# Optimization experiments

Measured on AMD Instinct MI355X. Metric: run time of the kernel, lower is better.

## Reference

```python
import jax, jax.numpy as jnp
import numpy as np
from jax import lax

H = W = 224
FH = FW = 7          # backbone feature map spatial size
THRESH = 0.7
NUM_CLASSES = 14


def _conv(x, w, stride, pad):
    return lax.conv_general_dilated(
        x, w, (stride, stride), [(pad, pad), (pad, pad)],
        dimension_numbers=('NCHW', 'OIHW', 'NCHW'))


def backbone(x, w0, w1, w2, w3, fw, fb):
    # stand-in resnet50 trunk: 224 -> 56 -> 28 -> 14 -> 7, channels 3->64->512->1024->2048
    h = jax.nn.relu(_conv(x, w0, 4, 3))      # [B,64,56,56]
    h = jax.nn.relu(_conv(h, w1, 2, 1))      # [B,512,28,28]
    h = jax.nn.relu(_conv(h, w2, 2, 1))      # [B,1024,14,14]
    feat = jax.nn.relu(_conv(h, w3, 2, 1))   # [B,2048,7,7]
    pool = feat.max(axis=(2, 3))             # MaxPool2d(k=7,s=1) on 7x7 == global max -> [B,2048]
    out = jax.nn.sigmoid(pool @ fw.T + fb)   # fc + Sigmoid -> [B,14]
    return out, feat, pool


def attention_gen_patchs(img, fm):
    B, C, Hh, Ww = img.shape
    # per-sample channel-max abs heatmap, min-max normalized
    hm = jnp.max(jnp.abs(fm), axis=1)                              # [B,7,7]
    mn = hm.min(axis=(1, 2), keepdims=True)
    mx = hm.max(axis=(1, 2), keepdims=True)
    hm = (hm - mn) / (mx - mn)
    hm = jax.image.resize(hm, (B, Hh, Ww), method='bilinear')      # Resize((h,w))
    mask = (hm > THRESH).astype(jnp.int32)                         # [B,H,W]

    # largest 8-connected component: iterative max-label propagation
    ids = jnp.arange(1, Hh * Ww + 1, dtype=jnp.int32).reshape(1, Hh, Ww) * mask
    def body(_, lab):
        p = lax.reduce_window(lab, jnp.int32(0), lax.max, (1, 3, 3), (1, 1, 1), 'SAME')
        return p * mask
    labels = lax.fori_loop(0, Hh + Ww, body, ids)                  # [B,H,W] int32

    def counts_one(lab):
        c = jnp.zeros((Hh * Ww + 1,), jnp.int32).at[lab.reshape(-1)].add(1)
        return c.at[0].set(-1)                                     # ignore background
    counts = jax.vmap(counts_one)(labels)                          # [B,H*W+1]
    max_label = jnp.argmax(counts, axis=1)                         # [B]
    lcc = labels == max_label[:, None, None]                       # [B,H,W] bool

    # bbox of largest component (xmin/xmax over rows, ymin/ymax over cols)
    ri = jnp.arange(Hh); ci = jnp.arange(Ww)
    rows = lcc.any(axis=2); cols = lcc.any(axis=1)
    xmin = jnp.min(jnp.where(rows, ri[None, :], Hh), axis=1)
    xmax = jnp.max(jnp.where(rows, ri[None, :], -1), axis=1)       # inclusive; torch slice excludes it
    ymin = jnp.min(jnp.where(cols, ci[None, :], Ww), axis=1)
    ymax = jnp.max(jnp.where(cols, ci[None, :], -1), axis=1)
    ch = jnp.maximum(xmax - xmin, 1).astype(jnp.float32)           # crop height (exclusive slice)
    cw = jnp.maximum(ymax - ymin, 1).astype(jnp.float32)

    # bilinear resize of crop [xmin:xmax, ymin:ymax] back to (H,W), align_corners=False
    fy0 = xmin.astype(jnp.float32); fx0 = ymin.astype(jnp.float32)
    oy = (jnp.arange(Hh, dtype=jnp.float32) + 0.5)[None, :] * (ch[:, None] / Hh) + fy0[:, None] - 0.5
    ox = (jnp.arange(Ww, dtype=jnp.float32) + 0.5)[None, :] * (cw[:, None] / Ww) + fx0[:, None] - 0.5
    oy = jnp.clip(oy, fy0[:, None], jnp.maximum(fy0 + ch - 1.0, fy0)[:, None])
    ox = jnp.clip(ox, fx0[:, None], jnp.maximum(fx0 + cw - 1.0, fx0)[:, None])

    def sample_one(im, yy, xx):  # im [C,H,W]
        gy = jnp.broadcast_to(yy[:, None], (Hh, Ww))
        gx = jnp.broadcast_to(xx[None, :], (Hh, Ww))
        f = lambda chan: jax.scipy.ndimage.map_coordinates(chan, [gy, gx], order=1, mode='nearest')
        return jax.vmap(f)(im)
    return jax.vmap(sample_one)(img, oy, ox)                       # [B,C,H,W]


def bce(p, t):
    p = jnp.clip(p, 1e-7, 1.0 - 1e-7)
    return -jnp.mean(t * jnp.log(p) + (1.0 - t) * jnp.log1p(-p))


def setup_inputs() -> dict:
    key = jax.random.key(0)
    ks = jax.random.split(key, 20)
    B = 4
    def conv_w(k, o, i, s):
        return jax.random.normal(k, (o, i, s, s), jnp.float32) * np.sqrt(2.0 / (i * s * s)).astype(np.float32)
    def lin(k, o, i):
        return jax.random.normal(k, (o, i), jnp.float32) * np.sqrt(1.0 / i).astype(np.float32)
    inp = {
        'img': jax.random.uniform(ks[0], (B, 3, H, W), jnp.float32),
        'target': jax.random.uniform(ks[1], (B, NUM_CLASSES), jnp.float32),
        'gw0': conv_w(ks[2], 64, 3, 7), 'gw1': conv_w(ks[3], 512, 64, 3),
        'gw2': conv_w(ks[4], 1024, 512, 3), 'gw3': conv_w(ks[5], 2048, 1024, 3),
        'gfw': lin(ks[6], NUM_CLASSES, 2048), 'gfb': jnp.zeros((NUM_CLASSES,), jnp.float32),
        'lw0': conv_w(ks[7], 64, 3, 7), 'lw1': conv_w(ks[8], 512, 64, 3),
        'lw2': conv_w(ks[9], 1024, 512, 3), 'lw3': conv_w(ks[10], 2048, 1024, 3),
        'lfw': lin(ks[11], NUM_CLASSES, 2048), 'lfb': jnp.zeros((NUM_CLASSES,), jnp.float32),
        'fw': lin(ks[12], NUM_CLASSES, 2048 * 2), 'fb': jnp.zeros((NUM_CLASSES,), jnp.float32),
    }
    return inp


def reference(img, target, gw0, gw1, gw2, gw3, gfw, gfb,
              lw0, lw1, lw2, lw3, lfw, lfb, fw, fb):
    out_g, fm_g, pool_g = backbone(img, gw0, gw1, gw2, gw3, gfw, gfb)
    # patch generation is non-differentiable in the original (CPU/PIL round trip)
    patch = attention_gen_patchs(lax.stop_gradient(img), lax.stop_gradient(fm_g))
    out_l, _, pool_l = backbone(patch, lw0, lw1, lw2, lw3, lfw, lfb)
    out_f = jax.nn.sigmoid(jnp.concatenate([pool_g, pool_l], axis=1) @ fw.T + fb)
    gl = bce(out_g, target); ll = bce(out_l, target); fl = bce(out_f, target)
    loss = 0.8 * gl + 0.1 * ll + 0.1 * fl
    return loss, out_g, out_l, out_f, patch
```

## Files before the change

### kernel.cpp

```cpp
#include <hip/hip_runtime.h>
#include <math.h>

typedef __attribute__((ext_vector_type(8))) short short8m;
typedef __attribute__((ext_vector_type(4))) float f32x4;

__device__ inline unsigned short bf16_trunc(float f) {
  return (unsigned short)(__float_as_uint(f) >> 16);
}
__device__ inline unsigned short bf16_rte(float f) {
  unsigned u = __float_as_uint(f);
  u += 0x7fffu + ((u >> 16) & 1u);
  return (unsigned short)(u >> 16);
}
__device__ inline float bf16_tof(unsigned short h) {
  return __uint_as_float(((unsigned)h) << 16);
}
__device__ inline short8m* ldsPtr(unsigned short* base, int row, int byteInRow) {
  int off = (row * 128 + byteInRow) ^ ((row & 7) << 4);
  return (short8m*)((char*)base + off);
}
__device__ inline void gload16_lds(const void* g, void* d) {
  __builtin_amdgcn_global_load_lds((const __attribute__((address_space(1))) unsigned int*)g,
                                   (__attribute__((address_space(3))) unsigned int*)d, 16, 0, 0);
}

__global__ __launch_bounds__(256) void k_conv7(const float* __restrict__ x,
                                               const float* __restrict__ w,
                                               float* __restrict__ y) {
  __shared__ float ws[147];
  const int boc = blockIdx.y;
  const int oc = boc & 63;
  const int b = boc >> 6;
  for (int i = threadIdx.x; i < 147; i += 256) ws[i] = w[oc * 147 + i];
  __syncthreads();
  int px = blockIdx.x * 256 + threadIdx.x;
  if (px >= 56 * 56) return;
  int oy = px / 56, ox = px % 56;
  int iy0 = oy * 4 - 3, ix0 = ox * 4 - 3;
  float acc = 0.f;
  for (int c = 0; c < 3; ++c) {
    const float* xp = x + ((size_t)(b * 3 + c)) * 224 * 224;
    #pragma unroll
    for (int ky = 0; ky < 7; ++ky) {
      int iy = iy0 + ky;
      if ((unsigned)iy < 224u) {
        #pragma unroll
        for (int kx = 0; kx < 7; ++kx) {
          int ix = ix0 + kx;
          if ((unsigned)ix < 224u)
            acc += xp[iy * 224 + ix] * ws[c * 49 + ky * 7 + kx];
        }
      }
    }
  }
  y[((size_t)boc * 56 + oy) * 56 + ox] = fmaxf(acc, 0.f);
}

__global__ __launch_bounds__(256) void k_padw(const float* __restrict__ w,
                                              float* __restrict__ wp,
                                              int kreal, int ktot, int noc) {
  int i = blockIdx.x * 256 + threadIdx.x;
  if (i >= noc * ktot) return;
  int oc = i / ktot, k = i % ktot;
  wp[i] = (k < kreal) ? w[oc * kreal + k] : 0.f;
}

template <int CIN, int HIN, int WIN, int HOUT, int WOUT, int KH, int KW, int STR, int PAD, int KTOT>
__global__ __launch_bounds__(256) void k_im2col(const float* __restrict__ x,
                                                unsigned short* __restrict__ XgH,
                                                unsigned short* __restrict__ XgM) {
  constexpr int NPX = 4 * HOUT * WOUT;
  constexpr int K8 = KTOT / 8;
  constexpr int KK = KH * KW;
  int u = blockIdx.x * 256 + threadIdx.x;
  int pxin = u & 63;
  int k8 = (u >> 6) % K8;
  int pxblk = (u >> 6) / K8;
  int px = pxblk * 64 + pxin;
  if (px > NPX - 1) px = NPX - 1;
  const int hw = HOUT * WOUT;
  int pbv = px / hw;
  int r = px % hw;
  int py = r / WOUT, pxv = r % WOUT;
  short8m ph, pm;
  #pragma unroll
  for (int i = 0; i < 8; ++i) {
    int k = k8 * 8 + i;
    int ci = k / KK, tap = k - ci * KK;
    float v = 0.f;
    if (ci < CIN) {
      int iy = py * STR - PAD + tap / KW, ix = pxv * STR - PAD + (tap % KW);
      if ((unsigned)iy < (unsigned)HIN && (unsigned)ix < (unsigned)WIN)
        v = x[(((size_t)pbv * CIN + ci) * HIN + iy) * WIN + ix];
    }
    unsigned short hb = bf16_trunc(v);
    unsigned short mb = bf16_rte(v - bf16_tof(hb));
    ph[i] = (short)hb; pm[i] = (short)mb;
  }
  size_t off = (size_t)u * 8;
  *(short8m*)(XgH + off) = ph;
  *(short8m*)(XgM + off) = pm;
}

template <int COUT, int HOUT, int WOUT, int KTOT, int SPLIT>
__global__ __launch_bounds__(256) void k_gemmx(const unsigned short* __restrict__ XgH,
                                               const unsigned short* __restrict__ XgM,
                                               const float* __restrict__ wsrc,
                                               float* __restrict__ part) {
  constexpr int NPX = 4 * HOUT * WOUT;
  constexpr int NPXB = (NPX + 63) / 64;
  constexpr int NOCB = COUT / 64;
  constexpr int NWG = NPXB * NOCB * SPLIT;
  constexpr int KCH = KTOT / SPLIT;
  constexpr int NCH = KCH / 64;
  __shared__ __align__(16) unsigned short XsH[4096];
  __shared__ __align__(16) unsigned short XsM[4096];
  __shared__ __align__(16) unsigned short WsH[4096];
  __shared__ __align__(16) unsigned short WsM[4096];
  __shared__ int pb[64], pyA[64], pxA[64];
  const int tid = threadIdx.x;
  const int flat = blockIdx.x;
  constexpr int q = NWG >> 3, r = NWG & 7;
  const int xc = flat & 7, of = flat >> 3;
  const int work = ((xc < r) ? xc * (q + 1) : r * (q + 1) + (xc - r) * q) + of;
  const int pxblk = work % NPXB;
  const int t2 = work / NPXB;
  const int oc0 = (t2 % NOCB) * 64;
  const int spl = t2 / NOCB;
  if (tid < 64) {
    int p = pxblk * 64 + tid;
    if (p > NPX - 1) p = NPX - 1;
    int hw = HOUT * WOUT;
    pb[tid] = p / hw;
    int rr = p % hw;
    pyA[tid] = rr / WOUT;
    pxA[tid] = rr % WOUT;
  }
  f32x4 acc[4] = {};
  const int l = tid & 63, wv = tid >> 6;
  const int lr = l & 15, lh = l >> 4;
  __syncthreads();
  for (int ch = 0; ch < NCH; ++ch) {
    const int kbase = spl * KCH + ch * 64;
    const size_t tileOff = (size_t)pxblk * KTOT * 64 + (size_t)kbase * 64;
    #pragma unroll
    for (int t = 0; t < 4; ++t) {
      int ins = wv * 4 + t;
      int pl = ins >> 3, ko = ins & 7;
      const unsigned short* g = (pl ? XgM : XgH) + tileOff + ko * 512 + l * 8;
      unsigned short* d = (pl ? XsM : XsH) + ko * 512;
      gload16_lds(g, d);
    }
    #pragma unroll
    for (int j = 0; j < 2; ++j) {
      int c = tid + 256 * j;
      int oc = c >> 3, koct = c & 7;
      const float* wp = wsrc + (size_t)(oc0 + oc) * KTOT + kbase + koct * 8;
      float vv[8];
      *(float4*)&vv[0] = *(const float4*)wp;
      *(float4*)&vv[4] = *(const float4*)(wp + 4);
      short8m ph, pm;
      #pragma unroll
      for (int i = 0; i < 8; ++i) {
        unsigned short hb = bf16_trunc(vv[i]);
        unsigned short mb = bf16_rte(vv[i] - bf16_tof(hb));
        ph[i] = (short)hb; pm[i] = (short)mb;
      }
      *ldsPtr(WsH, oc, koct * 16) = ph;
      *ldsPtr(WsM, oc, koct * 16) = pm;
    }
    __syncthreads();
    #pragma unroll
    for (int ks = 0; ks < 2; ++ks) {
      const int kbyte = ks * 64 + lh * 16;
      short8m aH = *ldsPtr(WsH, wv * 16 + lr, kbyte);
      short8m aM = *ldsPtr(WsM, wv * 16 + lr, kbyte);
      const int xoff = (ks * 4 + lh) * 512;
      #pragma unroll
      for (int g4 = 0; g4 < 4; ++g4) {
        short8m bH = *(const short8m*)(XsH + xoff + (g4 * 16 + lr) * 8);
        short8m bM = *(const short8m*)(XsM + xoff + (g4 * 16 + lr) * 8);
        acc[g4] = __builtin_amdgcn_mfma_f32_16x16x32_bf16(aH, bH, acc[g4], 0, 0, 0);
        acc[g4] = __builtin_amdgcn_mfma_f32_16x16x32_bf16(aH, bM, acc[g4], 0, 0, 0);
        acc[g4] = __builtin_amdgcn_mfma_f32_16x16x32_bf16(aM, bH, acc[g4], 0, 0, 0);
      }
    }
    __syncthreads();
  }
  const size_t N = (size_t)4 * COUT * HOUT * WOUT;
  #pragma unroll
  for (int g4 = 0; g4 < 4; ++g4) {
    int pxl = g4 * 16 + lr;
    int pidx = pxblk * 64 + pxl;
    if (pidx < NPX) {
      #pragma unroll
      for (int rr = 0; rr < 4; ++rr) {
        int ocl = wv * 16 + lh * 4 + rr;
        float v = acc[g4][rr];
        if (SPLIT == 1) v = fmaxf(v, 0.f);
        part[(size_t)spl * N +
             (((size_t)pb[pxl] * COUT + (oc0 + ocl)) * HOUT + pyA[pxl]) * WOUT + pxA[pxl]] = v;
      }
    }
  }
}

template <int CIN, int HIN, int WIN, int COUT, int HOUT, int WOUT, int SPLIT>
__global__ __launch_bounds__(256) void k_convm(const float* __restrict__ x,
                                               const float* __restrict__ wsrc,
                                               float* __restrict__ part) {
  constexpr int NPX = 4 * HOUT * WOUT;
  constexpr int KTOT = (CIN * 9) / SPLIT;
  constexpr int NCH = KTOT / 64;
  __shared__ __align__(16) unsigned short Xs[2][64][64];
  __shared__ __align__(16) unsigned short Wsh[3][64][64];
  __shared__ int pb[64], pyA[64], pxA[64];
  const int tid = threadIdx.x;
  const int oc0 = blockIdx.y * 64, px0 = blockIdx.x * 64;
  const int spl = blockIdx.z;
  const int kg0 = spl * KTOT;
  if (tid < 64) {
    int p = px0 + tid;
    if (p > NPX - 1) p = NPX - 1;
    int hw = HOUT * WOUT;
    pb[tid] = p / hw;
    int r = p % hw;
    pyA[tid] = r / WOUT;
    pxA[tid] = r % WOUT;
  }
  f32x4 acc[4] = {};
  const int l = tid & 63, wv = tid >> 6;
  const int lr = l & 15, lh = l >> 4;
  __syncthreads();
  for (int ch = 0; ch < NCH; ++ch) {
    const int kbase = kg0 + ch * 64;
    #pragma unroll
    for (int j = 0; j < 2; ++j) {
      int c = tid + 256 * j;
      int oc = c >> 3, koct = c & 7;
      const float* wp = wsrc + (size_t)(oc0 + oc) * (CIN * 9) + kbase + koct * 8;
      float vv[8];
      *(float4*)&vv[0] = *(const float4*)wp;
      *(float4*)&vv[4] = *(const float4*)(wp + 4);
      short8m ph, pm, pl2;
      #pragma unroll
      for (int i = 0; i < 8; ++i) {
        unsigned short hb = bf16_trunc(vv[i]);
        float r = vv[i] - bf16_tof(hb);
        unsigned short mb = bf16_rte(r);
        float r2 = r - bf16_tof(mb);
        unsigned short lb = bf16_rte(r2);
        ph[i] = (short)hb; pm[i] = (short)mb; pl2[i] = (short)lb;
      }
      *ldsPtr(&Wsh[0][0][0], oc, koct * 16) = ph;
      *ldsPtr(&Wsh[1][0][0], oc, koct * 16) = pm;
      *ldsPtr(&Wsh[2][0][0], oc, koct * 16) = pl2;
    }
    #pragma unroll
    for (int j = 0; j < 2; ++j) {
      int c = tid + 256 * j;
      int px = c & 63, koct = c >> 6;
      int pbv = pb[px], py = pyA[px], pxv = pxA[px];
      float vv[8];
      #pragma unroll
      for (int i = 0; i < 8; ++i) {
        int k = kbase + koct * 8 + i;
        int ci = k / 9, tap = k - ci * 9;
        int iy = py * 2 - 1 + tap / 3, ix = pxv * 2 - 1 + (tap % 3);
        float v = 0.f;
        if ((unsigned)iy < (unsigned)HIN && (unsigned)ix < (unsigned)WIN)
          v = x[(((size_t)pbv * CIN + ci) * HIN + iy) * WIN + ix];
        vv[i] = v;
      }
      short8m ph, pm;
      #pragma unroll
      for (int i = 0; i < 8; ++i) {
        unsigned short hb = bf16_trunc(vv[i]);
        unsigned short mb = bf16_rte(vv[i] - bf16_tof(hb));
        ph[i] = (short)hb; pm[i] = (short)mb;
      }
      *ldsPtr(&Xs[0][0][0], px, koct * 16) = ph;
      *ldsPtr(&Xs[1][0][0], px, koct * 16) = pm;
    }
    __syncthreads();
    #pragma unroll
    for (int ks = 0; ks < 2; ++ks) {
      const int kbyte = ks * 64 + lh * 16;
      short8m aH = *ldsPtr(&Wsh[0][0][0], wv * 16 + lr, kbyte);
      short8m aM = *ldsPtr(&Wsh[1][0][0], wv * 16 + lr, kbyte);
      short8m aL = *ldsPtr(&Wsh[2][0][0], wv * 16 + lr, kbyte);
      #pragma unroll
      for (int g = 0; g < 4; ++g) {
        short8m bH = *ldsPtr(&Xs[0][0][0], g * 16 + lr, kbyte);
        short8m bM = *ldsPtr(&Xs[1][0][0], g * 16 + lr, kbyte);
        acc[g] = __builtin_amdgcn_mfma_f32_16x16x32_bf16(aH, bH, acc[g], 0, 0, 0);
        acc[g] = __builtin_amdgcn_mfma_f32_16x16x32_bf16(aH, bM, acc[g], 0, 0, 0);
        acc[g] = __builtin_amdgcn_mfma_f32_16x16x32_bf16(aM, bH, acc[g], 0, 0, 0);
        acc[g] = __builtin_amdgcn_mfma_f32_16x16x32_bf16(aM, bM, acc[g], 0, 0, 0);
        acc[g] = __builtin_amdgcn_mfma_f32_16x16x32_bf16(aL, bH, acc[g], 0, 0, 0);
      }
    }
    __syncthreads();
  }
  const size_t N = (size_t)4 * COUT * HOUT * WOUT;
  #pragma unroll
  for (int g = 0; g < 4; ++g) {
    int pxl = g * 16 + lr;
    int pidx = px0 + pxl;
    if (pidx < NPX) {
      #pragma unroll
      for (int r = 0; r < 4; ++r) {
        int ocl = wv * 16 + lh * 4 + r;
        part[(size_t)spl * N +
             (((size_t)pb[pxl] * COUT + (oc0 + ocl)) * HOUT + pyA[pxl]) * WOUT + pxA[pxl]] =
            acc[g][r];
      }
    }
  }
}

template <int SPLIT>
__global__ __launch_bounds__(256) void k_red(const float* __restrict__ part,
                                             float* __restrict__ y, int n) {
  for (int i = blockIdx.x * 256 + threadIdx.x; i < n; i += gridDim.x * 256) {
    float s = 0.f;
    #pragma unroll
    for (int sp = 0; sp < SPLIT; ++sp) s += part[(size_t)sp * n + i];
    y[i] = fmaxf(s, 0.f);
  }
}

__global__ __launch_bounds__(256) void k_pool(const float* __restrict__ feat,
                                              float* __restrict__ pool) {
  int idx = blockIdx.x * 256 + threadIdx.x;
  if (idx >= 8192) return;
  const float* fp = feat + (size_t)idx * 49;
  float m = fp[0];
  #pragma unroll
  for (int i = 1; i < 49; ++i) m = fmaxf(m, fp[i]);
  pool[idx] = m;
}

__global__ __launch_bounds__(256) void k_fcsig(const float* __restrict__ pool,
                                               const float* __restrict__ fw,
                                               const float* __restrict__ fb,
                                               float* __restrict__ outp) {
  __shared__ float red[256];
  const int blk = blockIdx.x;
  const int b = blk / 14, c = blk % 14;
  const int tid = threadIdx.x;
  float s = 0.f;
  for (int k = tid; k < 2048; k += 256) s += pool[b * 2048 + k] * fw[c * 2048 + k];
  red[tid] = s;
  __syncthreads();
  for (int st = 128; st > 0; st >>= 1) {
    if (tid < st) red[tid] += red[tid + st];
    __syncthreads();
  }
  if (tid == 0) outp[b * 14 + c] = 1.f / (1.f + expf(-(red[0] + fb[c])));
}

__global__ __launch_bounds__(256) void k_fcsig2(const float* __restrict__ poolg,
                                                const float* __restrict__ pooll,
                                                const float* __restrict__ fw,
                                                const float* __restrict__ fb,
                                                float* __restrict__ outp) {
  __shared__ float red[256];
  const int blk = blockIdx.x;
  const int b = blk / 14, c = blk % 14;
  const int tid = threadIdx.x;
  const float* w = fw + (size_t)c * 4096;
  float s = 0.f;
  for (int k = tid; k < 2048; k += 256) s += poolg[b * 2048 + k] * w[k];
  for (int k = tid; k < 2048; k += 256) s += pooll[b * 2048 + k] * w[2048 + k];
  red[tid] = s;
  __syncthreads();
  for (int st = 128; st > 0; st >>= 1) {
    if (tid < st) red[tid] += red[tid + st];
    __syncthreads();
  }
  if (tid == 0) outp[blk] = 1.f / (1.f + expf(-(red[0] + fb[c])));
}

__global__ __launch_bounds__(64) void k_loss(const float* __restrict__ target,
                                             float* __restrict__ dout) {
  __shared__ float red[64];
  const int tid = threadIdx.x;
  float term = 0.f;
  if (tid < 56) {
    float t = target[tid];
    float pg = dout[1 + tid], plo = dout[57 + tid], pf = dout[113 + tid];
    auto bce1 = [&](float pp) {
      pp = fminf(fmaxf(pp, 1e-7f), 1.f - 1e-7f);
      return -(t * logf(pp) + (1.f - t) * log1pf(-pp));
    };
    term = (0.8f * bce1(pg) + 0.1f * bce1(plo) + 0.1f * bce1(pf)) * (1.f / 56.f);
  }
  red[tid] = term;
  __syncthreads();
  for (int st = 32; st > 0; st >>= 1) {
    if (tid < st) red[tid] += red[tid + st];
    __syncthreads();
  }
  if (tid == 0) dout[0] = red[0];
}

__global__ __launch_bounds__(256) void k_hm7a(const float* __restrict__ feat,
                                              float* __restrict__ hmr) {
  __shared__ float red[256];
  const int b = blockIdx.x / 49, cell = blockIdx.x % 49;
  const int tid = threadIdx.x;
  float m = 0.f;
  for (int ch = tid; ch < 2048; ch += 256)
    m = fmaxf(m, fabsf(feat[((size_t)b * 2048 + ch) * 49 + cell]));
  red[tid] = m;
  __syncthreads();
  for (int st = 128; st > 0; st >>= 1) {
    if (tid < st) red[tid] = fmaxf(red[tid], red[tid + st]);
    __syncthreads();
  }
  if (tid == 0) hmr[b * 49 + cell] = red[0];
}

__global__ __launch_bounds__(64) void k_hm7b(const float* __restrict__ hmr,
                                             float* __restrict__ hm7) {
  __shared__ float h[49];
  const int b = blockIdx.x, tid = threadIdx.x;
  if (tid < 49) h[tid] = hmr[b * 49 + tid];
  __syncthreads();
  if (tid == 0) {
    float mn = h[0], mx = h[0];
    for (int i = 1; i < 49; ++i) {
      mn = fminf(mn, h[i]);
      mx = fmaxf(mx, h[i]);
    }
    for (int i = 0; i < 49; ++i) hm7[b * 49 + i] = (h[i] - mn) / (mx - mn);
  }
}

#define MAXR 8
#define NRUNS (224 * MAXR)
__global__ __launch_bounds__(256) void k_ccl(const float* __restrict__ hm7, float* __restrict__ bbox) {
  const int b = blockIdx.x, tid = threadIdx.x;
  __shared__ float h7[49];
  __shared__ short rx0[NRUNS], rx1[NRUNS];
  __shared__ short nr[224];
  __shared__ int lab[NRUNS];
  __shared__ int cnt[NRUNS], mid[NRUNS];
  __shared__ int rmn[NRUNS], rmx[NRUNS], cmn[NRUNS], cmx[NRUNS];
  __shared__ int chg, chg2;
  __shared__ int bestC[256], bestM[256], bestI[256];

  if (tid < 49) h7[tid] = hm7[b * 49 + tid];
  for (int i = tid; i < NRUNS; i += 256) {
    cnt[i] = 0; mid[i] = -1;
    rmn[i] = 1 << 30; rmx[i] = -1; cmn[i] = 1 << 30; cmx[i] = -1;
    lab[i] = i;
  }
  __syncthreads();
  if (tid < 224) {
    int yy = tid;
    float py = ((float)yy + 0.5f) * (7.f / 224.f) - 0.5f;
    py = fminf(fmaxf(py, 0.f), 6.f);
    int y0 = (int)floorf(py);
    if (y0 > 5) y0 = 5;
    float fy = py - (float)y0;
    int n = 0, start = -1;
    const int segLo[6] = {0, 48, 80, 112, 144, 176};
    const int segHi[6] = {48, 80, 112, 144, 176, 224};
    #pragma unroll
    for (int s = 0; s < 6; ++s) {
      float A = h7[y0 * 7 + s], B = h7[y0 * 7 + s + 1];
      float C = h7[(y0 + 1) * 7 + s], D = h7[(y0 + 1) * 7 + s + 1];
      for (int xx = segLo[s]; xx < segHi[s]; ++xx) {
        float px = ((float)xx + 0.5f) * (7.f / 224.f) - 0.5f;
        px = fminf(fmaxf(px, 0.f), 6.f);
        float fx = px - (float)s;
        float v = (1.f - fy) * ((1.f - fx) * A + fx * B) +
                  fy * ((1.f - fx) * C + fx * D);
        bool m = v > 0.7f;
        if (m && start < 0) start = xx;
        if (!m && start >= 0) {
          if (n < MAXR) { rx0[yy * MAXR + n] = (short)start; rx1[yy * MAXR + n] = (short)(xx - 1); n++; }
          start = -1;
        }
      }
    }
    if (start >= 0 && n < MAXR) { rx0[yy * MAXR + n] = (short)start; rx1[yy * MAXR + n] = 223; n++; }
    nr[yy] = (short)n;
  }
  __syncthreads();
  int myA0[7], myA1[7];
  bool myV[7];
  #pragma unroll
  for (int j = 0; j < 7; ++j) {
    int i = tid + j * 256;
    int yy = i >> 3, k = i & 7;
    bool v = (k < (int)nr[yy]);
    myV[j] = v;
    myA0[j] = v ? (int)rx0[i] : 0;
    myA1[j] = v ? (int)rx1[i] : 0;
  }
  for (int outer = 0; outer < 48; ++outer) {
    if (tid == 0) chg = 0;
    __syncthreads();
    bool any = false;
    #pragma unroll
    for (int j = 0; j < 7; ++j) {
      if (!myV[j]) continue;
      int i = tid + j * 256;
      int yy = i >> 3;
      int a0 = myA0[j], a1 = myA1[j];
      int ri = lab[i];
      if (yy > 0) {
        int n1 = nr[yy - 1];
        for (int kk = 0; kk < n1; ++kk) {
          int q = ((yy - 1) << 3) + kk;
          if (a0 <= rx1[q] + 1 && a1 >= rx0[q] - 1) {
            int rq = lab[q];
            if (rq < ri) { atomicMin(&lab[ri], rq); any = true; }
            else if (ri < rq) { atomicMin(&lab[rq], ri); any = true; }
          }
        }
      }
      if (yy < 223) {
        int n1 = nr[yy + 1];
        for (int kk = 0; kk < n1; ++kk) {
          int q = ((yy + 1) << 3) + kk;
          if (a0 <= rx1[q] + 1 && a1 >= rx0[q] - 1) {
            int rq = lab[q];
            if (rq < ri) { atomicMin(&lab[ri], rq); any = true; }
            else if (ri < rq) { atomicMin(&lab[rq], ri); any = true; }
          }
        }
      }
    }
    if (any) chg = 1;
    __syncthreads();
    for (int sc = 0; sc < 12; ++sc) {
      if (tid == 0) chg2 = 0;
      __syncthreads();
      bool a2 = false;
      #pragma unroll
      for (int j = 0; j < 7; ++j) {
        int i = tid + j * 256;
        int ll = lab[i];
        int l2 = lab[ll];
        if (l2 < ll) { lab[i] = l2; a2 = true; }
      }
      if (a2) chg2 = 1;
      __syncthreads();
      if (!chg2) break;
    }
    if (!chg) break;
  }
  for (int i = tid; i < NRUNS; i += 256) {
    int yy = i >> 3, k = i & 7;
    if (k >= (int)nr[yy]) continue;
    int r = lab[i];
    int a0 = rx0[i], a1 = rx1[i];
    atomicAdd(&cnt[r], a1 - a0 + 1);
    atomicMax(&mid[r], yy * 224 + a1 + 1);
    atomicMin(&rmn[r], yy);
    atomicMax(&rmx[r], yy);
    atomicMin(&cmn[r], a0);
    atomicMax(&cmx[r], a1);
  }
  __syncthreads();
  int bc = -1, bm = 0x7fffffff, bi = -1;
  for (int i = tid; i < NRUNS; i += 256) {
    if (cnt[i] > 0 && lab[i] == i) {
      if (cnt[i] > bc || (cnt[i] == bc && mid[i] < bm)) { bc = cnt[i]; bm = mid[i]; bi = i; }
    }
  }
  bestC[tid] = bc; bestM[tid] = bm; bestI[tid] = bi;
  __syncthreads();
  for (int st = 128; st > 0; st >>= 1) {
    if (tid < st) {
      if (bestC[tid + st] > bestC[tid] ||
          (bestC[tid + st] == bestC[tid] && bestM[tid + st] < bestM[tid])) {
        bestC[tid] = bestC[tid + st]; bestM[tid] = bestM[tid + st]; bestI[tid] = bestI[tid + st];
      }
    }
    __syncthreads();
  }
  if (tid == 0) {
    int bw = bestI[0];
    float fy0, chf, fx0, cwf;
    if (bw < 0) { fy0 = 224.f; chf = 1.f; fx0 = 224.f; cwf = 1.f; }
    else {
      int dr = rmx[bw] - rmn[bw]; if (dr < 1) dr = 1;
      int dc = cmx[bw] - cmn[bw]; if (dc < 1) dc = 1;
      fy0 = (float)rmn[bw]; chf = (float)dr;
      fx0 = (float)cmn[bw]; cwf = (float)dc;
    }
    bbox[b * 4 + 0] = fy0; bbox[b * 4 + 1] = chf;
    bbox[b * 4 + 2] = fx0; bbox[b * 4 + 3] = cwf;
  }
}

__global__ __launch_bounds__(256) void k_sample(const float* __restrict__ img,
                                                const float* __restrict__ bbox,
                                                float* __restrict__ patch_out,
                                                float* __restrict__ patch_ws) {
  int idx = blockIdx.x * 256 + threadIdx.x;
  if (idx >= 4 * 3 * 224 * 224) return;
  int b = idx / (3 * 224 * 224);
  int r = idx % (3 * 224 * 224);
  int c = r / (224 * 224);
  int p = r % (224 * 224);
  int oy = p / 224, ox = p % 224;
  float fy0 = bbox[b * 4 + 0], chf = bbox[b * 4 + 1];
  float fx0 = bbox[b * 4 + 2], cwf = bbox[b * 4 + 3];
  float gy = ((float)oy + 0.5f) * (chf / 224.f) + fy0 - 0.5f;
  float gx = ((float)ox + 0.5f) * (cwf / 224.f) + fx0 - 0.5f;
  gy = fminf(fmaxf(gy, fy0), fmaxf(fy0 + chf - 1.f, fy0));
  gx = fminf(fmaxf(gx, fx0), fmaxf(fx0 + cwf - 1.f, fx0));
  int y0 = (int)floorf(gy);
  int x0 = (int)floorf(gx);
  float fy = gy - (float)y0, fx = gx - (float)x0;
  int y0c = min(max(y0, 0), 223), y1c = min(max(y0 + 1, 0), 223);
  int x0c = min(max(x0, 0), 223), x1c = min(max(x0 + 1, 0), 223);
  const float* ip = img + ((size_t)b * 3 + c) * 224 * 224;
  float v00 = ip[y0c * 224 + x0c], v01 = ip[y0c * 224 + x1c];
  float v10 = ip[y1c * 224 + x0c], v11 = ip[y1c * 224 + x1c];
  float v = (1.f - fy) * ((1.f - fx) * v00 + fx * v01) + fy * ((1.f - fx) * v10 + fx * v11);
  patch_out[idx] = v;
  patch_ws[idx] = v;
}

extern "C" void kernel_launch(void* const* d_in, const int* in_sizes, int n_in,
                              void* d_out, int out_size, void* d_ws, size_t ws_size,
                              hipStream_t stream) {
  const float* img = (const float*)d_in[0];
  const float* target = (const float*)d_in[1];
  const float* gw0 = (const float*)d_in[2];
  const float* gw1 = (const float*)d_in[3];
  const float* gw2 = (const float*)d_in[4];
  const float* gw3 = (const float*)d_in[5];
  const float* gfw = (const float*)d_in[6];
  const float* gfb = (const float*)d_in[7];
  const float* lw0 = (const float*)d_in[8];
  const float* lw1 = (const float*)d_in[9];
  const float* lw2 = (const float*)d_in[10];
  const float* lw3 = (const float*)d_in[11];
  const float* lfw = (const float*)d_in[12];
  const float* lfb = (const float*)d_in[13];
  const float* fw = (const float*)d_in[14];
  const float* fb = (const float*)d_in[15];
  float* out = (float*)d_out;
  float* ws = (float*)d_ws;

  float* c1 = ws;
  float* c2 = c1 + 802816;
  float* c3 = c2 + 1605632;
  float* c4 = c3 + 802816;
  float* poolg = c4 + 401408;
  float* pooll = poolg + 8192;
  float* hm7 = pooll + 8192;
  float* hmr = hm7 + 196;
  float* bbox = hmr + 196;
  float* patch = ws + 3629568;
  float* part = ws + 4231680;
  float* Wp = part + 2800000;
  unsigned short* XgH = (unsigned short*)(ws + 7442944);
  unsigned short* XgM = XgH + 3840000;

  const bool fast = ws_size >= (size_t)45131776;

  dim3 g7(13, 256);
  const int rg2 = 2048, rg3 = 2048, rg4 = 1568;

  for (int pass = 0; pass < 2; ++pass) {
    const float* w0 = pass ? lw0 : gw0;
    const float* w1 = pass ? lw1 : gw1;
    const float* w2 = pass ? lw2 : gw2;
    const float* w3 = pass ? lw3 : gw3;
    const float* fwp = pass ? lfw : gfw;
    const float* fbp = pass ? lfb : gfb;
    const float* inp = pass ? patch : img;
    float* pool = pass ? pooll : poolg;
    float* outp = pass ? (out + 57) : (out + 1);

    if (fast) {
      k_padw<<<48, 256, 0, stream>>>(w0, Wp, 147, 192, 64);
      k_im2col<3, 224, 224, 56, 56, 7, 7, 4, 3, 192><<<1176, 256, 0, stream>>>(inp, XgH, XgM);
      k_gemmx<64, 56, 56, 192, 1><<<196, 256, 0, stream>>>(XgH, XgM, Wp, c1);
      k_im2col<64, 56, 56, 28, 28, 3, 3, 2, 1, 576><<<882, 256, 0, stream>>>(c1, XgH, XgM);
      k_gemmx<512, 28, 28, 576, 1><<<392, 256, 0, stream>>>(XgH, XgM, w1, c2);
      k_im2col<512, 28, 28, 14, 14, 3, 3, 2, 1, 4608><<<1872, 256, 0, stream>>>(c2, XgH, XgM);
      k_gemmx<1024, 14, 14, 4608, 4><<<832, 256, 0, stream>>>(XgH, XgM, w2, part);
      k_red<4><<<rg3, 256, 0, stream>>>(part, c3, 802816);
      k_im2col<1024, 14, 14, 7, 7, 3, 3, 2, 1, 9216><<<1152, 256, 0, stream>>>(c3, XgH, XgM);
      k_gemmx<2048, 7, 7, 9216, 8><<<1024, 256, 0, stream>>>(XgH, XgM, w3, part);
      k_red<8><<<rg4, 256, 0, stream>>>(part, c4, 401408);
    } else {
      k_conv7<<<g7, 256, 0, stream>>>(inp, w0, c1);
      k_convm<64, 56, 56, 512, 28, 28, 1><<<dim3(49, 8, 1), 256, 0, stream>>>(c1, w1, part);
      k_red<1><<<rg2, 256, 0, stream>>>(part, c2, 1605632);
      k_convm<512, 28, 28, 1024, 14, 14, 4><<<dim3(13, 16, 4), 256, 0, stream>>>(c2, w2, part);
      k_red<4><<<rg3, 256, 0, stream>>>(part, c3, 802816);
      k_convm<1024, 14, 14, 2048, 7, 7, 8><<<dim3(4, 32, 8), 256, 0, stream>>>(c3, w3, part);
      k_red<8><<<rg4, 256, 0, stream>>>(part, c4, 401408);
    }
    k_pool<<<32, 256, 0, stream>>>(c4, pool);
    k_fcsig<<<56, 256, 0, stream>>>(pool, fwp, fbp, outp);

    if (pass == 0) {
      k_hm7a<<<196, 256, 0, stream>>>(c4, hmr);
      k_hm7b<<<4, 64, 0, stream>>>(hmr, hm7);
      k_ccl<<<4, 256, 0, stream>>>(hm7, bbox);
      k_sample<<<2352, 256, 0, stream>>>(img, bbox, out + 169, patch);
    }
  }
  k_fcsig2<<<56, 256, 0, stream>>>(poolg, pooll, fw, fb, out + 113);
  k_loss<<<1, 64, 0, stream>>>(target, out);
}
```

Baseline: 358.1 us.

## Double-buffer activation tiles and load weights directly into registers in k_gemmx

The GEMM kernel now double-buffers the activation LDS tiles, prefetching the next K-chunk with global_load_lds while the current one feeds MFMAs. Each lane loads only the fp32 weights its own MFMA A-fragment needs straight into registers and splits them into bf16 hi/lo there, so the weight LDS buffers and one barrier per chunk go away. Output index decoding moves from shared arrays to per-lane arithmetic. The cost is more registers (two 16-float weight buffers) and weight global loads that are no longer shared across the workgroup, which may reduce coalescing.

New measurement: 406.0 us. 1.13x slower.

```diff
diff --git a/kernel.cpp b/kernel.cpp
--- a/kernel.cpp
+++ b/kernel.cpp
@@ -113,11 +113,7 @@
   constexpr int NWG = NPXB * NOCB * SPLIT;
   constexpr int KCH = KTOT / SPLIT;
   constexpr int NCH = KCH / 64;
-  __shared__ __align__(16) unsigned short XsH[4096];
-  __shared__ __align__(16) unsigned short XsM[4096];
-  __shared__ __align__(16) unsigned short WsH[4096];
-  __shared__ __align__(16) unsigned short WsM[4096];
-  __shared__ int pb[64], pyA[64], pxA[64];
+  __shared__ __align__(16) unsigned short Xs[2][2][4096];
   const int tid = threadIdx.x;
   const int flat = blockIdx.x;
   constexpr int q = NWG >> 3, r = NWG & 7;
@@ -127,79 +123,97 @@
   const int t2 = work / NPXB;
   const int oc0 = (t2 % NOCB) * 64;
   const int spl = t2 / NOCB;
-  if (tid < 64) {
-    int p = pxblk * 64 + tid;
-    if (p > NPX - 1) p = NPX - 1;
-    int hw = HOUT * WOUT;
-    pb[tid] = p / hw;
-    int rr = p % hw;
-    pyA[tid] = rr / WOUT;
-    pxA[tid] = rr % WOUT;
-  }
   f32x4 acc[4] = {};
   const int l = tid & 63, wv = tid >> 6;
   const int lr = l & 15, lh = l >> 4;
-  __syncthreads();
-  for (int ch = 0; ch < NCH; ++ch) {
-    const int kbase = spl * KCH + ch * 64;
-    const size_t tileOff = (size_t)pxblk * KTOT * 64 + (size_t)kbase * 64;
+  const size_t tileBase = (size_t)pxblk * KTOT * 64 + (size_t)spl * KCH * 64;
+  const float* wrow = wsrc + (size_t)(oc0 + wv * 16 + lr) * KTOT + spl * KCH + lh * 8;
+
+  float wraw[16], wnext[16];
+  {
+    const size_t tOff = tileBase;
     #pragma unroll
     for (int t = 0; t < 4; ++t) {
       int ins = wv * 4 + t;
       int pl = ins >> 3, ko = ins & 7;
-      const unsigned short* g = (pl ? XgM : XgH) + tileOff + ko * 512 + l * 8;
-      unsigned short* d = (pl ? XsM : XsH) + ko * 512;
-      gload16_lds(g, d);
-    }
-    #pragma unroll
-    for (int j = 0; j < 2; ++j) {
-      int c = tid + 256 * j;
-      int oc = c >> 3, koct = c & 7;
-      const float* wp = wsrc + (size_t)(oc0 + oc) * KTOT + kbase + koct * 8;
-      float vv[8];
-      *(float4*)&vv[0] = *(const float4*)wp;
-      *(float4*)&vv[4] = *(const float4*)(wp + 4);
-      short8m ph, pm;
+      const unsigned short* g = (pl ? XgM : XgH) + tOff + ko * 512 + l * 8;
+      gload16_lds(g, &Xs[0][pl][ko * 512]);
+    }
+    const float* p = wrow;
+    *(float4*)&wraw[0] = *(const float4*)p;
+    *(float4*)&wraw[4] = *(const float4*)(p + 4);
+    *(float4*)&wraw[8] = *(const float4*)(p + 32);
+    *(float4*)&wraw[12] = *(const float4*)(p + 36);
+  }
+  asm volatile("s_waitcnt vmcnt(0)" ::: "memory");
+  __builtin_amdgcn_s_barrier();
+  __builtin_amdgcn_sched_barrier(0);
+
+  int cur = 0;
+  for (int ch = 0; ch < NCH; ++ch) {
+    if (ch + 1 < NCH) {
+      const size_t tOff = tileBase + (size_t)(ch + 1) * 64 * 64;
+      #pragma unroll
+      for (int t = 0; t < 4; ++t) {
+        int ins = wv * 4 + t;
+        int pl = ins >> 3, ko = ins & 7;
+        const unsigned short* g = (pl ? XgM : XgH) + tOff + ko * 512 + l * 8;
+        gload16_lds(g, &Xs[cur ^ 1][pl][ko * 512]);
+      }
+      const float* p = wrow + (ch + 1) * 64;
+      *(float4*)&wnext[0] = *(const float4*)p;
+      *(float4*)&wnext[4] = *(const float4*)(p + 4);
+      *(float4*)&wnext[8] = *(const float4*)(p + 32);
+      *(float4*)&wnext[12] = *(const float4*)(p + 36);
+    }
+    short8m aH[2], aM[2];
+    #pragma unroll
+    for (int ks = 0; ks < 2; ++ks)
       #pragma unroll
       for (int i = 0; i < 8; ++i) {
-        unsigned short hb = bf16_trunc(vv[i]);
-        unsigned short mb = bf16_rte(vv[i] - bf16_tof(hb));
-        ph[i] = (short)hb; pm[i] = (short)mb;
-      }
-      *ldsPtr(WsH, oc, koct * 16) = ph;
-      *ldsPtr(WsM, oc, koct * 16) = pm;
-    }
-    __syncthreads();
+        float v = wraw[ks * 8 + i];
+        unsigned short hb = bf16_trunc(v);
+        unsigned short mb = bf16_rte(v - bf16_tof(hb));
+        aH[ks][i] = (short)hb; aM[ks][i] = (short)mb;
+      }
     #pragma unroll
     for (int ks = 0; ks < 2; ++ks) {
-      const int kbyte = ks * 64 + lh * 16;
-      short8m aH = *ldsPtr(WsH, wv * 16 + lr, kbyte);
-      short8m aM = *ldsPtr(WsM, wv * 16 + lr, kbyte);
       const int xoff = (ks * 4 + lh) * 512;
       #pragma unroll
       for (int g4 = 0; g4 < 4; ++g4) {
-        short8m bH = *(const short8m*)(XsH + xoff + (g4 * 16 + lr) * 8);
-        short8m bM = *(const short8m*)(XsM + xoff + (g4 * 16 + lr) * 8);
-        acc[g4] = __builtin_amdgcn_mfma_f32_16x16x32_bf16(aH, bH, acc[g4], 0, 0, 0);
-        acc[g4] = __builtin_amdgcn_mfma_f32_16x16x32_bf16(aH, bM, acc[g4], 0, 0, 0);
-        acc[g4] = __builtin_amdgcn_mfma_f32_16x16x32_bf16(aM, bH, acc[g4], 0, 0, 0);
-      }
-    }
-    __syncthreads();
-  }
+        short8m bH = *(const short8m*)(&Xs[cur][0][xoff + (g4 * 16 + lr) * 8]);
+        short8m bM = *(const short8m*)(&Xs[cur][1][xoff + (g4 * 16 + lr) * 8]);
+        acc[g4] = __builtin_amdgcn_mfma_f32_16x16x32_bf16(aH[ks], bH, acc[g4], 0, 0, 0);
+        acc[g4] = __builtin_amdgcn_mfma_f32_16x16x32_bf16(aH[ks], bM, acc[g4], 0, 0, 0);
+        acc[g4] = __builtin_amdgcn_mfma_f32_16x16x32_bf16(aM[ks], bH, acc[g4], 0, 0, 0);
+      }
+    }
+    asm volatile("s_waitcnt vmcnt(0)" ::: "memory");
+    __builtin_amdgcn_s_barrier();
+    __builtin_amdgcn_sched_barrier(0);
+    if (ch + 1 < NCH) {
+      #pragma unroll
+      for (int i = 0; i < 16; ++i) wraw[i] = wnext[i];
+    }
+    cur ^= 1;
+  }
+  const int hw = HOUT * WOUT;
   const size_t N = (size_t)4 * COUT * HOUT * WOUT;
   #pragma unroll
   for (int g4 = 0; g4 < 4; ++g4) {
     int pxl = g4 * 16 + lr;
     int pidx = pxblk * 64 + pxl;
     if (pidx < NPX) {
+      int pbv = pidx / hw;
+      int rr0 = pidx % hw;
+      int py = rr0 / WOUT, pxv = rr0 % WOUT;
       #pragma unroll
       for (int rr = 0; rr < 4; ++rr) {
         int ocl = wv * 16 + lh * 4 + rr;
         float v = acc[g4][rr];
         if (SPLIT == 1) v = fmaxf(v, 0.f);
         part[(size_t)spl * N +
-             (((size_t)pb[pxl] * COUT + (oc0 + ocl)) * HOUT + pyA[pxl]) * WOUT + pxA[pxl]] = v;
+             (((size_t)pbv * COUT + (oc0 + ocl)) * HOUT + py) * WOUT + pxv] = v;
       }
     }
   }
```
